# Kernel optimization log

Hardware: AMD Instinct MI355X
Metric: run time of the kernel (lower is better)

## Reference

```python
import jax, jax.numpy as jnp
import numpy as np

B, S, HID = 2, 2048, 2048
H, KVH, D = 16, 4, 128
GROUPS = H // KVH  # 4


def apply_rotary(x, cos, sin):
    # x: [B, h, S, D]; cos/sin: [S, D//2]
    xr = x[..., 0::2]
    xi = x[..., 1::2]
    c = cos[None, None, :, :]
    s = sin[None, None, :, :]
    orr = xr * c - xi * s
    oi = xr * s + xi * c
    return jnp.stack([orr, oi], axis=-1).reshape(x.shape)


def setup_inputs() -> dict:
    key = jax.random.key(0)
    k0, k1, k2, k3, k4 = jax.random.split(key, 5)
    x = jax.random.normal(k0, (B, S, HID), dtype=jnp.float32)
    # real RoPE frequencies (llama-style), stored as [S, D//2, 2] = (cos, sin)
    inv_freq = 1.0 / (10000.0 ** (np.arange(0, D, 2, dtype=np.float32) / D))
    t = np.arange(S, dtype=np.float32)
    ang = np.outer(t, inv_freq)  # [S, D//2]
    freqs_cis = jnp.asarray(np.stack([np.cos(ang), np.sin(ang)], axis=-1), dtype=jnp.float32)
    sc = 0.02
    wq = jax.random.normal(k1, (HID, H * D), dtype=jnp.float32) * sc
    wk = jax.random.normal(k2, (HID, KVH * D), dtype=jnp.float32) * sc
    wv = jax.random.normal(k3, (HID, KVH * D), dtype=jnp.float32) * sc
    wo = jax.random.normal(k4, (H * D, HID), dtype=jnp.float32) * sc
    return {"x": x, "freqs_cis": freqs_cis, "wq": wq, "wk": wk, "wv": wv, "wo": wo}


def reference(x, freqs_cis, wq, wk, wv, wo):
    b, s, _ = x.shape
    cos, sin = freqs_cis[..., 0], freqs_cis[..., 1]
    q = (x @ wq).reshape(b, s, H, D).transpose(0, 2, 1, 3)    # [B,H,S,D]
    k = (x @ wk).reshape(b, s, KVH, D).transpose(0, 2, 1, 3)  # [B,KVH,S,D]
    v = (x @ wv).reshape(b, s, KVH, D).transpose(0, 2, 1, 3)
    q = apply_rotary(q, cos, sin)
    k = apply_rotary(k, cos, sin)
    # GQA expand: repeat kv heads into query-head groups
    k = jnp.repeat(k, GROUPS, axis=1)  # [B,H,S,D]
    v = jnp.repeat(v, GROUPS, axis=1)
    scale = 1.0 / jnp.sqrt(jnp.asarray(D, dtype=x.dtype))
    scores = jnp.einsum("bhqd,bhkd->bhqk", q, k) * scale
    causal = jnp.tril(jnp.ones((s, s), dtype=bool))
    scores = jnp.where(causal[None, None], scores, jnp.asarray(-jnp.inf, dtype=scores.dtype))
    attn = jax.nn.softmax(scores, axis=-1)
    out = jnp.einsum("bhqk,bhkd->bhqd", attn, v)
    out = out.transpose(0, 2, 1, 3).reshape(b, s, H * D)
    return out @ wo
```

## Files before the change

### kernel.cpp

```cpp
#include <hip/hip_runtime.h>
#include <hip/hip_bf16.h>

#define B_   2
#define S_   2048
#define HID_ 2048
#define H_   16
#define KVH_ 4
#define D_   128
#define M_   4096
#define NQKV 3072

typedef __attribute__((ext_vector_type(8))) short bf16x8;
typedef __attribute__((ext_vector_type(4))) float f32x4;
typedef __attribute__((ext_vector_type(16))) float f32x16;
typedef const __attribute__((address_space(1))) unsigned int* gas_p;
typedef __attribute__((address_space(3))) unsigned int* las_p;

__device__ __forceinline__ unsigned short f2b(float f) {
    __hip_bfloat16 h = __float2bfloat16(f);
    return *reinterpret_cast<unsigned short*>(&h);
}
__device__ __forceinline__ float b2f(unsigned short u) {
    __hip_bfloat16 h;
    *reinterpret_cast<unsigned short*>(&h) = u;
    return __bfloat162float(h);
}

__global__ __launch_bounds__(256)
void convert_x(const float* __restrict__ x, unsigned short* __restrict__ xb) {
    int i = (blockIdx.x * 256 + threadIdx.x) * 4;
    float4 v = *(const float4*)(x + i);
    ushort4 o;
    o.x = f2b(v.x); o.y = f2b(v.y); o.z = f2b(v.z); o.w = f2b(v.w);
    *(ushort4*)(xb + i) = o;
}

__global__ __launch_bounds__(256)
void convert_w_all(const float* __restrict__ wq, const float* __restrict__ wk,
                   const float* __restrict__ wv, const float* __restrict__ wo,
                   unsigned short* __restrict__ wqkvT,
                   unsigned short* __restrict__ woT) {
    __shared__ float tile[32][33];
    int z = blockIdx.z;
    const float* w; int N, nbase; unsigned short* dst;
    if (z == 0)      { w = wq; N = 2048; nbase = 0;    dst = wqkvT; }
    else if (z == 1) { w = wk; N = 512;  nbase = 2048; dst = wqkvT; }
    else if (z == 2) { w = wv; N = 512;  nbase = 2560; dst = wqkvT; }
    else             { w = wo; N = 2048; nbase = 0;    dst = woT; }
    int n0 = blockIdx.x * 32, k0 = blockIdx.y * 32;
    if (n0 >= N) return;
    int tx = threadIdx.x & 31, ty = threadIdx.x >> 5;
    #pragma unroll
    for (int j = 0; j < 4; j++)
        tile[ty + j*8][tx] = w[(size_t)(k0 + ty + j*8) * N + n0 + tx];
    __syncthreads();
    #pragma unroll
    for (int j = 0; j < 4; j++)
        dst[(size_t)(nbase + n0 + ty + j*8) * 2048 + k0 + tx] = f2b(tile[tx][ty + j*8]);
}

__global__ __launch_bounds__(256)
void gemm_qkv(const unsigned short* __restrict__ A,
              const unsigned short* __restrict__ BT,
              unsigned short* __restrict__ qkv,
              unsigned short* __restrict__ vT,
              const float* __restrict__ freqs) {
    __shared__ unsigned short As[128 * 64];
    __shared__ unsigned short Bs[128 * 64];

    int tid  = threadIdx.x;
    int lane = tid & 63, w = tid >> 6;
    int l31 = lane & 31, h = lane >> 5;
    int row0 = blockIdx.y * 128, col0 = blockIdx.x * 128;
    int wm = (w & 1) * 64, wn = (w >> 1) * 64;

    f32x16 acc[2][2];
    #pragma unroll
    for (int i = 0; i < 2; i++)
        #pragma unroll
        for (int j = 0; j < 2; j++)
            #pragma unroll
            for (int r = 0; r < 16; r++) acc[i][j][r] = 0.f;

    const unsigned short* Arow = A  + (size_t)row0 * 2048;
    const unsigned short* Brow = BT + (size_t)col0 * 2048;

    for (int k0 = 0; k0 < 2048; k0 += 64) {
        #pragma unroll
        for (int it = 0; it < 4; it++) {
            int c = w * 256 + it * 64 + lane;
            int r = c >> 3, qp = c & 7;
            int q8 = (qp ^ (r & 7)) * 8;
            __builtin_amdgcn_global_load_lds(
                (gas_p)(Arow + (size_t)r * 2048 + k0 + q8),
                (las_p)((char*)&As[0] + (size_t)(w * 256 + it * 64) * 16),
                16, 0, 0);
            __builtin_amdgcn_global_load_lds(
                (gas_p)(Brow + (size_t)r * 2048 + k0 + q8),
                (las_p)((char*)&Bs[0] + (size_t)(w * 256 + it * 64) * 16),
                16, 0, 0);
        }
        __syncthreads();
        #pragma unroll
        for (int kk = 0; kk < 4; kk++) {
            int chunk = kk * 2 + h;
            bf16x8 af[2], bf[2];
            #pragma unroll
            for (int i = 0; i < 2; i++) {
                int row = wm + i*32 + l31;
                af[i] = *(const bf16x8*)&As[row * 64 + (chunk ^ (row & 7)) * 8];
            }
            #pragma unroll
            for (int j = 0; j < 2; j++) {
                int row = wn + j*32 + l31;
                bf[j] = *(const bf16x8*)&Bs[row * 64 + (chunk ^ (row & 7)) * 8];
            }
            #pragma unroll
            for (int i = 0; i < 2; i++)
                #pragma unroll
                for (int j = 0; j < 2; j++)
                    acc[i][j] = __builtin_amdgcn_mfma_f32_32x32x16_bf16(af[i], bf[j], acc[i][j], 0, 0, 0);
        }
        __syncthreads();
    }

    bool isV = (col0 >= 2560);
    #pragma unroll
    for (int i = 0; i < 2; i++) {
        #pragma unroll
        for (int j = 0; j < 2; j++) {
            int colb = col0 + wn + j*32 + l31;
            if (!isV) {
                int dd = (colb & 127) & ~1;
                bool odd = colb & 1;
                #pragma unroll
                for (int rg = 0; rg < 4; rg++) {
                    int mbase = row0 + wm + i*32 + rg*8 + 4*h;
                    #pragma unroll
                    for (int rr = 0; rr < 4; rr++) {
                        int m = mbase + rr;
                        int s = m & 2047;
                        float v  = acc[i][j][rg*4 + rr];
                        float pv = __shfl_xor(v, 1);
                        float cs = freqs[s*128 + dd];
                        float sn = freqs[s*128 + dd + 1];
                        float o  = odd ? (pv*sn + v*cs) : (v*cs - pv*sn);
                        qkv[(size_t)m * NQKV + colb] = f2b(o);
                    }
                }
            } else {
                int vrow = (row0 >> 11) * 512 + (colb - 2560);
                #pragma unroll
                for (int rg = 0; rg < 4; rg++) {
                    int s0g = (row0 + wm + i*32 + rg*8 + 4*h) & 2047;
                    ushort4 ov;
                    ov.x = f2b(acc[i][j][rg*4 + 0]);
                    ov.y = f2b(acc[i][j][rg*4 + 1]);
                    ov.z = f2b(acc[i][j][rg*4 + 2]);
                    ov.w = f2b(acc[i][j][rg*4 + 3]);
                    *(ushort4*)(vT + (size_t)vrow * 2048 + s0g) = ov;
                }
            }
        }
    }
}

__global__ __launch_bounds__(256)
void gemm_out(const unsigned short* __restrict__ A,
              const unsigned short* __restrict__ BT,
              float* __restrict__ C, int N) {
    __shared__ unsigned short As[128 * 64];
    __shared__ unsigned short Bs[128 * 64];

    int tid  = threadIdx.x;
    int lane = tid & 63, w = tid >> 6;
    int l31 = lane & 31, h = lane >> 5;
    int row0 = blockIdx.y * 128, col0 = blockIdx.x * 128;
    int wm = (w & 1) * 64, wn = (w >> 1) * 64;

    f32x16 acc[2][2];
    #pragma unroll
    for (int i = 0; i < 2; i++)
        #pragma unroll
        for (int j = 0; j < 2; j++)
            #pragma unroll
            for (int r = 0; r < 16; r++) acc[i][j][r] = 0.f;

    const unsigned short* Arow = A  + (size_t)row0 * 2048;
    const unsigned short* Brow = BT + (size_t)col0 * 2048;

    for (int k0 = 0; k0 < 2048; k0 += 64) {
        #pragma unroll
        for (int it = 0; it < 4; it++) {
            int c = w * 256 + it * 64 + lane;
            int r = c >> 3, qp = c & 7;
            int q8 = (qp ^ (r & 7)) * 8;
            __builtin_amdgcn_global_load_lds(
                (gas_p)(Arow + (size_t)r * 2048 + k0 + q8),
                (las_p)((char*)&As[0] + (size_t)(w * 256 + it * 64) * 16),
                16, 0, 0);
            __builtin_amdgcn_global_load_lds(
                (gas_p)(Brow + (size_t)r * 2048 + k0 + q8),
                (las_p)((char*)&Bs[0] + (size_t)(w * 256 + it * 64) * 16),
                16, 0, 0);
        }
        __syncthreads();
        #pragma unroll
        for (int kk = 0; kk < 4; kk++) {
            int chunk = kk * 2 + h;
            bf16x8 af[2], bf[2];
            #pragma unroll
            for (int i = 0; i < 2; i++) {
                int row = wm + i*32 + l31;
                af[i] = *(const bf16x8*)&As[row * 64 + (chunk ^ (row & 7)) * 8];
            }
            #pragma unroll
            for (int j = 0; j < 2; j++) {
                int row = wn + j*32 + l31;
                bf[j] = *(const bf16x8*)&Bs[row * 64 + (chunk ^ (row & 7)) * 8];
            }
            #pragma unroll
            for (int i = 0; i < 2; i++)
                #pragma unroll
                for (int j = 0; j < 2; j++)
                    acc[i][j] = __builtin_amdgcn_mfma_f32_32x32x16_bf16(af[i], bf[j], acc[i][j], 0, 0, 0);
        }
        __syncthreads();
    }

    #pragma unroll
    for (int i = 0; i < 2; i++)
        #pragma unroll
        for (int j = 0; j < 2; j++) {
            int colb = col0 + wn + j*32 + l31;
            #pragma unroll
            for (int rg = 0; rg < 4; rg++) {
                int m = row0 + wm + i*32 + rg*8 + 4*h;
                #pragma unroll
                for (int rr = 0; rr < 4; rr++)
                    C[(size_t)(m + rr) * N + colb] = acc[i][j][rg*4 + rr];
            }
        }
}

__global__ __launch_bounds__(512)
void attn_mfma(const unsigned short* __restrict__ qkv,
               const unsigned short* __restrict__ vT,
               unsigned short* __restrict__ ao,
               unsigned short* __restrict__ wsP,
               float2* __restrict__ wsML) {
    __shared__ unsigned short Ks[64 * 128];
    __shared__ unsigned short Vt[128 * 64];

    int tid  = threadIdx.x;
    int lane = tid & 63, w = tid >> 6;
    int quad = lane >> 4, l15 = lane & 15;
    int hw = w >> 1, qhalf = w & 1;
    int bx = blockIdx.x, hk = blockIdx.y, b = blockIdx.z;
    int h = hk * 4 + hw;

    int qt, c;
    if (bx < 12)      { qt = 31 - bx / 3;        c = bx % 3; }
    else if (bx < 40) { qt = 27 - (bx - 12) / 2; c = (bx - 12) & 1; }
    else              { qt = 53 - bx;            c = 0; }
    int nt = qt + 1;
    int nch = (qt >= 28) ? 3 : (qt >= 14 ? 2 : 1);
    int kt_begin = c * 14;
    int kt_end = (nt < (c + 1) * 14) ? nt : (c + 1) * 14;
    bool lastc = (c == nch - 1);
    int q0 = qt * 64;
    const float scale = 0.08838834764831845f;

    bf16x8 aq[2][4];
    #pragma unroll
    for (int qf = 0; qf < 2; qf++) {
        const unsigned short* qrow =
            qkv + (size_t)(b*2048 + q0 + qhalf*32 + qf*16 + l15) * NQKV + h*128;
        #pragma unroll
        for (int k4 = 0; k4 < 4; k4++)
            aq[qf][k4] = *(const bf16x8*)(qrow + k4*32 + quad*8);
    }

    int koff[4][4];
    #pragma unroll
    for (int j = 0; j < 4; j++) {
        int row = ((j >> 1) * 32) + ((l15 >> 2) * 8) + ((j & 1) * 4) + (l15 & 3);
        #pragma unroll
        for (int k4 = 0; k4 < 4; k4++) {
            int slot = (k4 * 4 + quad) ^ (row & 15);
            koff[j][k4] = (row * 16 + slot) * 8;
        }
    }
    int vbase0 = (l15 * 8 + (quad ^ (l15 & 7))) * 8;
    int vbase1 = (l15 * 8 + ((4 + quad) ^ (l15 & 7))) * 8;

    const unsigned short* kb0 = qkv + (size_t)(b*2048) * NQKV + 2048 + hk*128;
    const unsigned short* vb0 = vT + (size_t)(b*512 + hk*128) * 2048;

    auto stage_k = [&](int kt) {
        #pragma unroll
        for (int it = 0; it < 2; it++) {
            int s = w * 128 + it * 64 + lane;
            int r = s >> 4, qp = s & 15;
            int q = qp ^ (r & 15);
            __builtin_amdgcn_global_load_lds(
                (gas_p)(kb0 + (size_t)(kt*64 + r) * NQKV + q * 8),
                (las_p)((char*)&Ks[0] + (w * 128 + it * 64) * 16),
                16, 0, 0);
        }
    };
    auto stage_v = [&](int kt) {
        #pragma unroll
        for (int it = 0; it < 2; it++) {
            int s = w * 128 + it * 64 + lane;
            int r = s >> 3, qp = s & 7;
            int q = qp ^ (r & 7);
            __builtin_amdgcn_global_load_lds(
                (gas_p)(vb0 + (size_t)r * 2048 + kt*64 + q * 8),
                (las_p)((char*)&Vt[0] + (w * 128 + it * 64) * 16),
                16, 0, 0);
        }
    };

    f32x4 o_acc[2][8];
    const f32x4 zf = {0.f, 0.f, 0.f, 0.f};
    #pragma unroll
    for (int qf = 0; qf < 2; qf++)
        #pragma unroll
        for (int jn = 0; jn < 8; jn++) o_acc[qf][jn] = zf;
    float m_i[2] = {-1e30f, -1e30f}, l_i[2] = {0.f, 0.f};
    int qglob[2] = {q0 + qhalf*32 + l15, q0 + qhalf*32 + 16 + l15};

    stage_k(kt_begin);
    for (int kt = kt_begin; kt < kt_end; kt++) {
        __syncthreads();
        stage_v(kt);

        f32x4 s_acc[2][4];
        #pragma unroll
        for (int j = 0; j < 4; j++) {
            s_acc[0][j] = zf; s_acc[1][j] = zf;
            #pragma unroll
            for (int k4 = 0; k4 < 4; k4++) {
                bf16x8 ak = *(const bf16x8*)&Ks[koff[j][k4]];
                s_acc[0][j] = __builtin_amdgcn_mfma_f32_16x16x32_bf16(ak, aq[0][k4], s_acc[0][j], 0, 0, 0);
                s_acc[1][j] = __builtin_amdgcn_mfma_f32_16x16x32_bf16(ak, aq[1][k4], s_acc[1][j], 0, 0, 0);
            }
        }

        bf16x8 pp[2][2];
        #pragma unroll
        for (int qf = 0; qf < 2; qf++) {
            float sv[4][4];
            #pragma unroll
            for (int j = 0; j < 4; j++)
                #pragma unroll
                for (int r = 0; r < 4; r++)
                    sv[j][r] = s_acc[qf][j][r] * scale;
            if (kt == qt) {
                #pragma unroll
                for (int j = 0; j < 4; j++)
                    #pragma unroll
                    for (int r = 0; r < 4; r++) {
                        int sloc = ((j >> 1) * 32) + quad*8 + ((j & 1) * 4) + r;
                        if (kt*64 + sloc > qglob[qf]) sv[j][r] = -1e30f;
                    }
            }
            float mx = sv[0][0];
            #pragma unroll
            for (int j = 0; j < 4; j++)
                #pragma unroll
                for (int r = 0; r < 4; r++) mx = fmaxf(mx, sv[j][r]);
            mx = fmaxf(mx, __shfl_xor(mx, 16));
            mx = fmaxf(mx, __shfl_xor(mx, 32));
            float mnew = fmaxf(m_i[qf], mx);
            float alpha = __expf(m_i[qf] - mnew);
            float rs = 0.f;
            float p[4][4];
            #pragma unroll
            for (int j = 0; j < 4; j++)
                #pragma unroll
                for (int r = 0; r < 4; r++) {
                    p[j][r] = __expf(sv[j][r] - mnew);
                    rs += p[j][r];
                }
            l_i[qf] = l_i[qf] * alpha + rs;
            m_i[qf] = mnew;
            #pragma unroll
            for (int jn = 0; jn < 8; jn++)
                #pragma unroll
                for (int r = 0; r < 4; r++) o_acc[qf][jn][r] *= alpha;
            #pragma unroll
            for (int r = 0; r < 4; r++) {
                pp[qf][0][r]     = (short)f2b(p[0][r]);
                pp[qf][0][r + 4] = (short)f2b(p[1][r]);
                pp[qf][1][r]     = (short)f2b(p[2][r]);
                pp[qf][1][r + 4] = (short)f2b(p[3][r]);
            }
        }

        __syncthreads();
        if (kt + 1 < kt_end) stage_k(kt + 1);

        #pragma unroll
        for (int jn = 0; jn < 8; jn++) {
            bf16x8 av0 = *(const bf16x8*)&Vt[jn*1024 + vbase0];
            bf16x8 av1 = *(const bf16x8*)&Vt[jn*1024 + vbase1];
            o_acc[0][jn] = __builtin_amdgcn_mfma_f32_16x16x32_bf16(av0, pp[0][0], o_acc[0][jn], 0, 0, 0);
            o_acc[0][jn] = __builtin_amdgcn_mfma_f32_16x16x32_bf16(av1, pp[0][1], o_acc[0][jn], 0, 0, 0);
            o_acc[1][jn] = __builtin_amdgcn_mfma_f32_16x16x32_bf16(av0, pp[1][0], o_acc[1][jn], 0, 0, 0);
            o_acc[1][jn] = __builtin_amdgcn_mfma_f32_16x16x32_bf16(av1, pp[1][1], o_acc[1][jn], 0, 0, 0);
        }
    }

    int pi = 0, mi = 0;
    if (qt >= 14) {
        if (qt < 28) { mi = (qt - 14) * 2 + c;       pi = qt - 14; }
        else         { mi = 28 + (qt - 28) * 3 + c;  pi = 14 + (qt - 28) * 2 + c; }
    }
    #pragma unroll
    for (int qf = 0; qf < 2; qf++) {
        float lt = l_i[qf];
        lt += __shfl_xor(lt, 16);
        lt += __shfl_xor(lt, 32);
        float inv = 1.f / lt;
        int q_local = qhalf * 32 + qf * 16 + l15;
        unsigned short* dst;
        if (lastc)
            dst = ao + (size_t)(b*2048 + q0 + q_local) * 2048 + h*128;
        else
            dst = wsP + (size_t)(((pi * 8 + hk * 2 + b) * 4 + hw) * 64 + q_local) * 128;
        #pragma unroll
        for (int jn = 0; jn < 8; jn++) {
            ushort4 ov;
            ov.x = f2b(o_acc[qf][jn][0] * inv);
            ov.y = f2b(o_acc[qf][jn][1] * inv);
            ov.z = f2b(o_acc[qf][jn][2] * inv);
            ov.w = f2b(o_acc[qf][jn][3] * inv);
            *(ushort4*)(dst + jn*16 + quad*4) = ov;
        }
        if (qt >= 14 && quad == 0)
            wsML[(mi * 8 + hk * 2 + b) * 256 + hw * 64 + q_local]
                = make_float2(m_i[qf], lt);
    }
}

__global__ __launch_bounds__(256)
void merge_kernel(unsigned short* __restrict__ ao,
                  const unsigned short* __restrict__ wsP,
                  const float2* __restrict__ wsML) {
    int t = blockIdx.x * 256 + threadIdx.x;
    int d = (t & 15) * 8;
    int h = (t >> 4) & 15;
    int rest = t >> 8;
    int q_off = rest % 1152;
    int b = rest / 1152;
    int q = 896 + q_off;
    int qt = q >> 6, q_local = q & 63;
    int hk = h >> 2, hw = h & 3;
    int nch = (qt >= 28) ? 3 : 2;

    float mv[3], lv[3];
    for (int cc = 0; cc < nch; cc++) {
        int mi = (qt < 28) ? (qt - 14) * 2 + cc : 28 + (qt - 28) * 3 + cc;
        float2 ml = wsML[(mi * 8 + hk * 2 + b) * 256 + hw * 64 + q_local];
        mv[cc] = ml.x; lv[cc] = ml.y;
    }
    float M = mv[0];
    for (int cc = 1; cc < nch; cc++) M = fmaxf(M, mv[cc]);
    float f[3], S = 0.f;
    for (int cc = 0; cc < nch; cc++) { f[cc] = __expf(mv[cc] - M) * lv[cc]; S += f[cc]; }
    float inv = 1.f / S;

    unsigned short* arow = ao + (size_t)(b*2048 + q) * 2048 + h*128 + d;
    float outv[8];
    {
        ushort4 a0 = *(ushort4*)arow, a1 = *(ushort4*)(arow + 4);
        float fl = f[nch-1];
        outv[0] = fl*b2f(a0.x); outv[1] = fl*b2f(a0.y);
        outv[2] = fl*b2f(a0.z); outv[3] = fl*b2f(a0.w);
        outv[4] = fl*b2f(a1.x); outv[5] = fl*b2f(a1.y);
        outv[6] = fl*b2f(a1.z); outv[7] = fl*b2f(a1.w);
    }
    for (int cc = 0; cc < nch - 1; cc++) {
        int pi = (qt < 28) ? (qt - 14) : 14 + (qt - 28) * 2 + cc;
        const unsigned short* prow =
            wsP + (size_t)(((pi * 8 + hk * 2 + b) * 4 + hw) * 64 + q_local) * 128 + d;
        ushort4 p0 = *(const ushort4*)prow, p1 = *(const ushort4*)(prow + 4);
        float fc = f[cc];
        outv[0] += fc*b2f(p0.x); outv[1] += fc*b2f(p0.y);
        outv[2] += fc*b2f(p0.z); outv[3] += fc*b2f(p0.w);
        outv[4] += fc*b2f(p1.x); outv[5] += fc*b2f(p1.y);
        outv[6] += fc*b2f(p1.z); outv[7] += fc*b2f(p1.w);
    }
    ushort4 o0, o1;
    o0.x = f2b(outv[0]*inv); o0.y = f2b(outv[1]*inv);
    o0.z = f2b(outv[2]*inv); o0.w = f2b(outv[3]*inv);
    o1.x = f2b(outv[4]*inv); o1.y = f2b(outv[5]*inv);
    o1.z = f2b(outv[6]*inv); o1.w = f2b(outv[7]*inv);
    *(ushort4*)arow = o0;
    *(ushort4*)(arow + 4) = o1;
}

extern "C" void kernel_launch(void* const* d_in, const int* in_sizes, int n_in,
                              void* d_out, int out_size, void* d_ws, size_t ws_size,
                              hipStream_t stream) {
    const float* x     = (const float*)d_in[0];
    const float* freqs = (const float*)d_in[1];
    const float* wq    = (const float*)d_in[2];
    const float* wk    = (const float*)d_in[3];
    const float* wv    = (const float*)d_in[4];
    const float* wo    = (const float*)d_in[5];
    float* out = (float*)d_out;

    char* ws = (char*)d_ws;
    unsigned short* xbf    = (unsigned short*)(ws);
    unsigned short* aobuf  = (unsigned short*)(ws);
    unsigned short* wqkvT  = (unsigned short*)(ws + (16u<<20));
    unsigned short* woT    = (unsigned short*)(ws + (28u<<20));
    unsigned short* qkvbuf = (unsigned short*)(ws + (36u<<20));
    unsigned short* vTbuf  = (unsigned short*)(ws + (60u<<20));
    unsigned short* wsP  = (unsigned short*)(ws + (16u<<20));
    float2*         wsML = (float2*)(ws + (16u<<20) + 176u*65536u);

    dim3 blk(256);
    convert_x<<<8192, blk, 0, stream>>>(x, xbf);
    convert_w_all<<<dim3(64, 64, 4), blk, 0, stream>>>(wq, wk, wv, wo, wqkvT, woT);
    gemm_qkv<<<dim3(NQKV/128, M_/128), blk, 0, stream>>>(xbf, wqkvT, qkvbuf, vTbuf, freqs);
    attn_mfma<<<dim3(54, 4, 2), dim3(512), 0, stream>>>(qkvbuf, vTbuf, aobuf, wsP, wsML);
    merge_kernel<<<2304, blk, 0, stream>>>(aobuf, wsP, wsML);
    gemm_out<<<dim3(2048/128, M_/128), blk, 0, stream>>>(aobuf, woT, out, 2048);
}
```

Measured before the change: 321.4 us.

## Replace QKV and output GEMMs with a 256x256 double-buffered pipelined 8-wave GEMM

Both projection GEMMs now go through a single kernel, gemm8. It uses 256x256 block tiles, 512 threads, a double-buffered LDS staging area and 16x16x32 bf16 MFMAs. The global-to-LDS loads for upcoming K tiles are interleaved with compute phases, gated by explicit vmcnt waits and barriers, and the MFMA phases run at raised wave priority. The aim is to hide load latency and raise arithmetic intensity compared with the old single-buffered 128x128 kernels. The trade-off is fewer blocks: 192 for QKV and 128 for the output GEMM, which may leave many CUs idle, plus more register pressure from 32 accumulator fragments.

```diff
diff --git a/kernel.cpp b/kernel.cpp
--- a/kernel.cpp
+++ b/kernel.cpp
@@ -59,188 +59,196 @@
         dst[(size_t)(nbase + n0 + ty + j*8) * 2048 + k0 + tx] = f2b(tile[tx][ty + j*8]);
 }
 
-__global__ __launch_bounds__(256)
-void gemm_qkv(const unsigned short* __restrict__ A,
-              const unsigned short* __restrict__ BT,
-              unsigned short* __restrict__ qkv,
-              unsigned short* __restrict__ vT,
-              const float* __restrict__ freqs) {
-    __shared__ unsigned short As[128 * 64];
-    __shared__ unsigned short Bs[128 * 64];
+#define BAR    asm volatile("s_barrier" ::: "memory")
+#define LG0    do { asm volatile("s_waitcnt lgkmcnt(0)" ::: "memory"); \
+                    __builtin_amdgcn_sched_barrier(0); } while (0)
+#define GATE6  asm volatile("s_waitcnt vmcnt(6)" ::: "memory")
+#define GATE0  asm volatile("s_waitcnt vmcnt(0)" ::: "memory")
+#define PHI    __builtin_amdgcn_s_setprio(1)
+#define PLO    __builtin_amdgcn_s_setprio(0)
+
+#define STG(srcrow, ldsbase, half, tile) do {                                   \
+    _Pragma("unroll")                                                           \
+    for (int it_ = 0; it_ < 2; ++it_) {                                         \
+      int p_ = w * 128 + it_ * 64 + lane;                                       \
+      int r_ = (half) * 128 + (p_ >> 3);                                        \
+      int q8_ = ((p_ & 7) ^ ((p_ >> 3) & 7)) * 8;                               \
+      __builtin_amdgcn_global_load_lds(                                         \
+          (gas_p)((srcrow) + (size_t)r_ * 2048 + (tile) * 64 + q8_),            \
+          (las_p)((char*)(ldsbase) + ((half) * 1024 + w * 128 + it_ * 64) * 16),\
+          16, 0, 0);                                                            \
+    } } while (0)
+
+#define RD_AF(bufi, mi) do {                                                    \
+    const unsigned short* Ab_ = &As[bufi][0] + (mi) * 8192 + wr * 4096 + l15 * 64; \
+    _Pragma("unroll")                                                           \
+    for (int f_ = 0; f_ < 4; ++f_) {                                            \
+      af[f_][0] = *(const bf16x8*)(Ab_ + f_ * 1024 + slot0);                    \
+      af[f_][1] = *(const bf16x8*)(Ab_ + f_ * 1024 + slot1);                    \
+    } } while (0)
+
+#define RD_BF(bufi, ni) do {                                                    \
+    const unsigned short* Bb_ = &Bs[bufi][0] + (ni) * 8192 + wc * 2048 + l15 * 64; \
+    _Pragma("unroll")                                                           \
+    for (int g_ = 0; g_ < 2; ++g_) {                                            \
+      bfr[ni][g_][0] = *(const bf16x8*)(Bb_ + g_ * 1024 + slot0);               \
+      bfr[ni][g_][1] = *(const bf16x8*)(Bb_ + g_ * 1024 + slot1);               \
+    } } while (0)
+
+#define MM(mi, ni) do {                                                         \
+    _Pragma("unroll")                                                           \
+    for (int f_ = 0; f_ < 4; ++f_)                                              \
+      _Pragma("unroll")                                                         \
+      for (int g_ = 0; g_ < 2; ++g_) {                                          \
+        acc[(mi)*4 + f_][(ni)*2 + g_] = __builtin_amdgcn_mfma_f32_16x16x32_bf16(\
+            af[f_][0], bfr[ni][g_][0], acc[(mi)*4 + f_][(ni)*2 + g_], 0, 0, 0); \
+        acc[(mi)*4 + f_][(ni)*2 + g_] = __builtin_amdgcn_mfma_f32_16x16x32_bf16(\
+            af[f_][1], bfr[ni][g_][1], acc[(mi)*4 + f_][(ni)*2 + g_], 0, 0, 0); \
+      } } while (0)
+
+__global__ __launch_bounds__(512)
+void gemm8(const unsigned short* __restrict__ A,
+           const unsigned short* __restrict__ BT,
+           int mode,
+           unsigned short* __restrict__ qkvb,
+           unsigned short* __restrict__ vTb,
+           const float* __restrict__ freqs,
+           float* __restrict__ Cf) {
+    __shared__ unsigned short As[2][16384];
+    __shared__ unsigned short Bs[2][16384];
 
     int tid  = threadIdx.x;
     int lane = tid & 63, w = tid >> 6;
-    int l31 = lane & 31, h = lane >> 5;
-    int row0 = blockIdx.y * 128, col0 = blockIdx.x * 128;
-    int wm = (w & 1) * 64, wn = (w >> 1) * 64;
-
-    f32x16 acc[2][2];
-    #pragma unroll
-    for (int i = 0; i < 2; i++)
-        #pragma unroll
-        for (int j = 0; j < 2; j++)
-            #pragma unroll
-            for (int r = 0; r < 16; r++) acc[i][j][r] = 0.f;
+    int l15  = lane & 15, quad = lane >> 4;
+    int wr = w >> 2, wc = w & 3;
+    int row0 = blockIdx.y * 256, col0 = blockIdx.x * 256;
+    int slot0 = (quad ^ (lane & 7)) * 8;
+    int slot1 = slot0 ^ 32;
 
     const unsigned short* Arow = A  + (size_t)row0 * 2048;
     const unsigned short* Brow = BT + (size_t)col0 * 2048;
 
-    for (int k0 = 0; k0 < 2048; k0 += 64) {
-        #pragma unroll
-        for (int it = 0; it < 4; it++) {
-            int c = w * 256 + it * 64 + lane;
-            int r = c >> 3, qp = c & 7;
-            int q8 = (qp ^ (r & 7)) * 8;
-            __builtin_amdgcn_global_load_lds(
-                (gas_p)(Arow + (size_t)r * 2048 + k0 + q8),
-                (las_p)((char*)&As[0] + (size_t)(w * 256 + it * 64) * 16),
-                16, 0, 0);
-            __builtin_amdgcn_global_load_lds(
-                (gas_p)(Brow + (size_t)r * 2048 + k0 + q8),
-                (las_p)((char*)&Bs[0] + (size_t)(w * 256 + it * 64) * 16),
-                16, 0, 0);
-        }
-        __syncthreads();
-        #pragma unroll
-        for (int kk = 0; kk < 4; kk++) {
-            int chunk = kk * 2 + h;
-            bf16x8 af[2], bf[2];
-            #pragma unroll
-            for (int i = 0; i < 2; i++) {
-                int row = wm + i*32 + l31;
-                af[i] = *(const bf16x8*)&As[row * 64 + (chunk ^ (row & 7)) * 8];
-            }
-            #pragma unroll
-            for (int j = 0; j < 2; j++) {
-                int row = wn + j*32 + l31;
-                bf[j] = *(const bf16x8*)&Bs[row * 64 + (chunk ^ (row & 7)) * 8];
-            }
-            #pragma unroll
-            for (int i = 0; i < 2; i++)
-                #pragma unroll
-                for (int j = 0; j < 2; j++)
-                    acc[i][j] = __builtin_amdgcn_mfma_f32_32x32x16_bf16(af[i], bf[j], acc[i][j], 0, 0, 0);
-        }
-        __syncthreads();
-    }
-
-    bool isV = (col0 >= 2560);
-    #pragma unroll
-    for (int i = 0; i < 2; i++) {
-        #pragma unroll
-        for (int j = 0; j < 2; j++) {
-            int colb = col0 + wn + j*32 + l31;
-            if (!isV) {
-                int dd = (colb & 127) & ~1;
-                bool odd = colb & 1;
-                #pragma unroll
-                for (int rg = 0; rg < 4; rg++) {
-                    int mbase = row0 + wm + i*32 + rg*8 + 4*h;
+    f32x4 acc[8][4];
+    #pragma unroll
+    for (int i = 0; i < 8; ++i)
+        #pragma unroll
+        for (int j = 0; j < 4; ++j) acc[i][j] = f32x4{0.f, 0.f, 0.f, 0.f};
+
+    bf16x8 af[4][2];
+    bf16x8 bfr[2][2][2];
+
+    STG(Arow, &As[0][0], 0, 0);
+    STG(Brow, &Bs[0][0], 0, 0);
+    STG(Arow, &As[0][0], 1, 0);
+    STG(Brow, &Bs[0][0], 1, 0);
+    STG(Arow, &As[1][0], 0, 1);
+    STG(Brow, &Bs[1][0], 0, 1);
+    STG(Brow, &Bs[1][0], 1, 1);
+    GATE6;
+    BAR;
+
+    #pragma unroll 1
+    for (int i = 0; i < 15; ++i) {
+        int t = 2 * i;
+        RD_AF(0, 0); RD_BF(0, 0); STG(Arow, &As[1][0], 1, t + 1);
+        BAR; LG0; PHI; MM(0, 0); PLO; BAR;
+        RD_BF(0, 1); STG(Arow, &As[0][0], 0, t + 2);
+        BAR; LG0; PHI; MM(0, 1); PLO; BAR;
+        RD_AF(0, 1); STG(Brow, &Bs[0][0], 0, t + 2);
+        BAR; LG0; PHI; MM(1, 0); PLO; BAR;
+        STG(Brow, &Bs[0][0], 1, t + 2);
+        BAR; LG0; PHI; MM(1, 1); PLO; GATE6; BAR;
+        RD_AF(1, 0); RD_BF(1, 0); STG(Arow, &As[0][0], 1, t + 2);
+        BAR; LG0; PHI; MM(0, 0); PLO; BAR;
+        RD_BF(1, 1); STG(Arow, &As[1][0], 0, t + 3);
+        BAR; LG0; PHI; MM(0, 1); PLO; BAR;
+        RD_AF(1, 1); STG(Brow, &Bs[1][0], 0, t + 3);
+        BAR; LG0; PHI; MM(1, 0); PLO; BAR;
+        STG(Brow, &Bs[1][0], 1, t + 3);
+        BAR; LG0; PHI; MM(1, 1); PLO; GATE6; BAR;
+    }
+    RD_AF(0, 0); RD_BF(0, 0); STG(Arow, &As[1][0], 1, 31);
+    BAR; LG0; PHI; MM(0, 0); PLO; BAR;
+    RD_BF(0, 1);
+    BAR; LG0; PHI; MM(0, 1); PLO; BAR;
+    RD_AF(0, 1);
+    BAR; LG0; PHI; MM(1, 0); PLO; BAR;
+    BAR; LG0; PHI; MM(1, 1); PLO; GATE0; BAR;
+    RD_AF(1, 0); RD_BF(1, 0);
+    BAR; LG0; PHI; MM(0, 0); PLO; BAR;
+    RD_BF(1, 1);
+    BAR; LG0; PHI; MM(0, 1); PLO; BAR;
+    RD_AF(1, 1);
+    BAR; LG0; PHI; MM(1, 0); PLO; BAR;
+    LG0; PHI; MM(1, 1); PLO;
+
+    int q4 = quad * 4;
+    if (mode == 0) {
+        if (col0 < 2560) {
+            #pragma unroll
+            for (int mi = 0; mi < 2; ++mi)
+            #pragma unroll
+            for (int f = 0; f < 4; ++f) {
+                int mb = row0 + mi*128 + wr*64 + f*16 + q4;
+                #pragma unroll
+                for (int ni = 0; ni < 2; ++ni)
+                #pragma unroll
+                for (int g = 0; g < 2; ++g) {
+                    int colb = col0 + ni*128 + wc*32 + g*16 + l15;
+                    int dd = (colb & 127) & ~1;
+                    bool odd = colb & 1;
                     #pragma unroll
-                    for (int rr = 0; rr < 4; rr++) {
-                        int m = mbase + rr;
+                    for (int rr = 0; rr < 4; ++rr) {
+                        int m = mb + rr;
                         int s = m & 2047;
-                        float v  = acc[i][j][rg*4 + rr];
+                        float v  = acc[mi*4 + f][ni*2 + g][rr];
                         float pv = __shfl_xor(v, 1);
                         float cs = freqs[s*128 + dd];
                         float sn = freqs[s*128 + dd + 1];
                         float o  = odd ? (pv*sn + v*cs) : (v*cs - pv*sn);
-                        qkv[(size_t)m * NQKV + colb] = f2b(o);
+                        qkvb[(size_t)m * NQKV + colb] = f2b(o);
                     }
                 }
-            } else {
-                int vrow = (row0 >> 11) * 512 + (colb - 2560);
-                #pragma unroll
-                for (int rg = 0; rg < 4; rg++) {
-                    int s0g = (row0 + wm + i*32 + rg*8 + 4*h) & 2047;
+            }
+        } else {
+            #pragma unroll
+            for (int mi = 0; mi < 2; ++mi)
+            #pragma unroll
+            for (int f = 0; f < 4; ++f) {
+                int mb = row0 + mi*128 + wr*64 + f*16 + q4;
+                int s0 = mb & 2047;
+                #pragma unroll
+                for (int ni = 0; ni < 2; ++ni)
+                #pragma unroll
+                for (int g = 0; g < 2; ++g) {
+                    int colb = col0 + ni*128 + wc*32 + g*16 + l15;
+                    int vrow = (row0 >> 11) * 512 + (colb - 2560);
                     ushort4 ov;
-                    ov.x = f2b(acc[i][j][rg*4 + 0]);
-                    ov.y = f2b(acc[i][j][rg*4 + 1]);
-                    ov.z = f2b(acc[i][j][rg*4 + 2]);
-                    ov.w = f2b(acc[i][j][rg*4 + 3]);
-                    *(ushort4*)(vT + (size_t)vrow * 2048 + s0g) = ov;
+                    ov.x = f2b(acc[mi*4 + f][ni*2 + g][0]);
+                    ov.y = f2b(acc[mi*4 + f][ni*2 + g][1]);
+                    ov.z = f2b(acc[mi*4 + f][ni*2 + g][2]);
+                    ov.w = f2b(acc[mi*4 + f][ni*2 + g][3]);
+                    *(ushort4*)(vTb + (size_t)vrow * 2048 + s0) = ov;
                 }
             }
         }
-    }
-}
-
-__global__ __launch_bounds__(256)
-void gemm_out(const unsigned short* __restrict__ A,
-              const unsigned short* __restrict__ BT,
-              float* __restrict__ C, int N) {
-    __shared__ unsigned short As[128 * 64];
-    __shared__ unsigned short Bs[128 * 64];
-
-    int tid  = threadIdx.x;
-    int lane = tid & 63, w = tid >> 6;
-    int l31 = lane & 31, h = lane >> 5;
-    int row0 = blockIdx.y * 128, col0 = blockIdx.x * 128;
-    int wm = (w & 1) * 64, wn = (w >> 1) * 64;
-
-    f32x16 acc[2][2];
-    #pragma unroll
-    for (int i = 0; i < 2; i++)
-        #pragma unroll
-        for (int j = 0; j < 2; j++)
-            #pragma unroll
-            for (int r = 0; r < 16; r++) acc[i][j][r] = 0.f;
-
-    const unsigned short* Arow = A  + (size_t)row0 * 2048;
-    const unsigned short* Brow = BT + (size_t)col0 * 2048;
-
-    for (int k0 = 0; k0 < 2048; k0 += 64) {
-        #pragma unroll
-        for (int it = 0; it < 4; it++) {
-            int c = w * 256 + it * 64 + lane;
-            int r = c >> 3, qp = c & 7;
-            int q8 = (qp ^ (r & 7)) * 8;
-            __builtin_amdgcn_global_load_lds(
-                (gas_p)(Arow + (size_t)r * 2048 + k0 + q8),
-                (las_p)((char*)&As[0] + (size_t)(w * 256 + it * 64) * 16),
-                16, 0, 0);
-            __builtin_amdgcn_global_load_lds(
-                (gas_p)(Brow + (size_t)r * 2048 + k0 + q8),
-                (las_p)((char*)&Bs[0] + (size_t)(w * 256 + it * 64) * 16),
-                16, 0, 0);
-        }
-        __syncthreads();
-        #pragma unroll
-        for (int kk = 0; kk < 4; kk++) {
-            int chunk = kk * 2 + h;
-            bf16x8 af[2], bf[2];
-            #pragma unroll
-            for (int i = 0; i < 2; i++) {
-                int row = wm + i*32 + l31;
-                af[i] = *(const bf16x8*)&As[row * 64 + (chunk ^ (row & 7)) * 8];
+    } else {
+        #pragma unroll
+        for (int mi = 0; mi < 2; ++mi)
+        #pragma unroll
+        for (int f = 0; f < 4; ++f) {
+            int mb = row0 + mi*128 + wr*64 + f*16 + q4;
+            #pragma unroll
+            for (int ni = 0; ni < 2; ++ni)
+            #pragma unroll
+            for (int g = 0; g < 2; ++g) {
+                int colb = col0 + ni*128 + wc*32 + g*16 + l15;
+                #pragma unroll
+                for (int rr = 0; rr < 4; ++rr)
+                    Cf[(size_t)(mb + rr) * 2048 + colb] = acc[mi*4 + f][ni*2 + g][rr];
             }
-            #pragma unroll
-            for (int j = 0; j < 2; j++) {
-                int row = wn + j*32 + l31;
-                bf[j] = *(const bf16x8*)&Bs[row * 64 + (chunk ^ (row & 7)) * 8];
-            }
-            #pragma unroll
-            for (int i = 0; i < 2; i++)
-                #pragma unroll
-                for (int j = 0; j < 2; j++)
-                    acc[i][j] = __builtin_amdgcn_mfma_f32_32x32x16_bf16(af[i], bf[j], acc[i][j], 0, 0, 0);
-        }
-        __syncthreads();
-    }
-
-    #pragma unroll
-    for (int i = 0; i < 2; i++)
-        #pragma unroll
-        for (int j = 0; j < 2; j++) {
-            int colb = col0 + wn + j*32 + l31;
-            #pragma unroll
-            for (int rg = 0; rg < 4; rg++) {
-                int m = row0 + wm + i*32 + rg*8 + 4*h;
-                #pragma unroll
-                for (int rr = 0; rr < 4; rr++)
-                    C[(size_t)(m + rr) * N + colb] = acc[i][j][rg*4 + rr];
-            }
-        }
+        }
+    }
 }
 
 __global__ __launch_bounds__(512)
@@ -526,8 +534,10 @@
     dim3 blk(256);
     convert_x<<<8192, blk, 0, stream>>>(x, xbf);
     convert_w_all<<<dim3(64, 64, 4), blk, 0, stream>>>(wq, wk, wv, wo, wqkvT, woT);
-    gemm_qkv<<<dim3(NQKV/128, M_/128), blk, 0, stream>>>(xbf, wqkvT, qkvbuf, vTbuf, freqs);
+    gemm8<<<dim3(NQKV/256, M_/256), dim3(512), 0, stream>>>(
+        xbf, wqkvT, 0, qkvbuf, vTbuf, freqs, nullptr);
     attn_mfma<<<dim3(54, 4, 2), dim3(512), 0, stream>>>(qkvbuf, vTbuf, aobuf, wsP, wsML);
     merge_kernel<<<2304, blk, 0, stream>>>(aobuf, wsP, wsML);
-    gemm_out<<<dim3(2048/128, M_/128), blk, 0, stream>>>(aobuf, woT, out, 2048);
-}
+    gemm8<<<dim3(2048/256, M_/256), dim3(512), 0, stream>>>(
+        aobuf, woT, 1, nullptr, nullptr, nullptr, out);
+}
```

After: 348.5 us. 8.5% more time.
